# Optimization experiments

Hardware: AMD Instinct MI355X
Metric: run time of the kernel (lower is better)

Reference implementation:

```python
import math
import jax, jax.numpy as jnp
import numpy as np

B, T, D, DFF, E, K = 2, 4096, 1024, 2048, 8, 2
CAP_FACTOR = 1.25


def setup_inputs() -> dict:
    key = jax.random.key(0)
    ks = jax.random.split(key, 5)
    x = jax.random.normal(ks[0], (B, T, D), dtype=jnp.float32)
    gate_w = jax.random.normal(ks[1], (E, D), dtype=jnp.float32) * 0.02
    W1 = jax.random.normal(ks[2], (E, D, DFF), dtype=jnp.float32) * 0.02
    b1 = jnp.zeros((E, DFF), dtype=jnp.float32)
    W2 = jax.random.normal(ks[3], (E, DFF, D), dtype=jnp.float32) * 0.02
    b2 = jnp.zeros((E, D), dtype=jnp.float32)
    return {"x": x, "gate_w": gate_w, "W1": W1, "b1": b1, "W2": W2, "b2": b2}


def _moe_forward(x, gate_w, W1, b1, W2, b2):
    Bs, Ts, Ds = x.shape
    N = Bs * Ts
    x_flat = x.reshape(N, Ds)

    # --- router ---
    logits = x_flat @ gate_w.T                          # (N, E)
    probs = jax.nn.softmax(logits, axis=-1)             # (N, E)
    top_w, top_i = jax.lax.top_k(probs, K)              # (N, K)
    disp_w = top_w / (jnp.sum(top_w, axis=-1, keepdims=True) + 1e-9)

    # --- capacity: slot-major, token-order priority (matches the Python loops) ---
    capacity = max(1, int(math.ceil(CAP_FACTOR * N * K / E)))
    idx_flat = top_i.T.reshape(-1)                       # (K*N,) slot-major order
    oh = jax.nn.one_hot(idx_flat, E, dtype=jnp.int32)    # (K*N, E)
    # position of each assignment within its expert's arrival order
    pos = jnp.sum(jnp.cumsum(oh, axis=0) * oh, axis=-1) - 1  # (K*N,)
    keep = (pos < capacity).reshape(K, N).T              # (N, K)
    w_capped = disp_w * keep.astype(disp_w.dtype)        # (N, K)

    # --- combine weights per expert ---
    oh_nke = jax.nn.one_hot(top_i, E, dtype=w_capped.dtype)   # (N, K, E)
    comb = jnp.einsum('nk,nke->ne', w_capped, oh_nke)         # (N, E)

    # --- experts: dense per-expert FFN, zero-weight tokens contribute nothing ---
    out = jnp.zeros_like(x_flat)
    for e in range(E):
        h = jax.nn.gelu(x_flat @ W1[e] + b1[e], approximate=False)  # (N, DFF)
        y = h @ W2[e] + b2[e]                                        # (N, D)
        out = out + comb[:, e:e + 1] * y

    # --- Switch-style aux load-balancing loss ---
    assigned = (jnp.sum(oh_nke, axis=1) > 0).astype(probs.dtype)  # (N, E)
    f = jnp.mean(assigned, axis=0)
    p = jnp.mean(probs, axis=0)
    aux_loss = E * jnp.sum(f * p)

    return out.reshape(Bs, Ts, Ds), aux_loss


def reference(x, gate_w, W1, b1, W2, b2):
    return _moe_forward(x, gate_w, W1, b1, W2, b2)
```

## Files before the change

### kernel.cpp

```cpp
#include <hip/hip_runtime.h>
#include <hip/hip_bf16.h>
#include <math.h>

#define NB   2
#define NT   4096
#define ND   1024
#define NDFF 2048
#define NE   8
#define NK   2
#define NN   (NB * NT)
#define NCAP 2560

typedef unsigned short ushort_t;
typedef __attribute__((ext_vector_type(8))) short bf16x8;
typedef __attribute__((ext_vector_type(8))) unsigned short u16x8;
typedef __attribute__((ext_vector_type(4))) float f32x4;

__device__ __forceinline__ float gelu_exact(float v) {
  return 0.5f * v * (1.0f + erff(v * 0.70710678118654752f));
}

__device__ __forceinline__ unsigned short f2bf(float f) {
  unsigned int u = __float_as_uint(f);
  u += 0x7fffu + ((u >> 16) & 1u);
  return (unsigned short)(u >> 16);
}
__device__ __forceinline__ float bf2f(unsigned short h) {
  return __uint_as_float(((unsigned int)h) << 16);
}

__device__ __forceinline__ void gl_lds16(const void* g, void* l) {
  __builtin_amdgcn_global_load_lds(
      (__attribute__((address_space(1))) void*)g,
      (__attribute__((address_space(3))) void*)l, 16, 0, 0);
}

__global__ __launch_bounds__(256) void router_kernel(
    const float* __restrict__ x, const float* __restrict__ gw,
    int* __restrict__ top_i, float* __restrict__ disp_w,
    float* __restrict__ p_sum, int* __restrict__ f_cnt) {
  __shared__ float s_p[NE];
  __shared__ int s_f[NE];
  if (threadIdx.x < NE) { s_p[threadIdx.x] = 0.0f; s_f[threadIdx.x] = 0; }
  __syncthreads();

  const int lane = threadIdx.x & 63;
  const int wv = threadIdx.x >> 6;
  const int n = blockIdx.x * 4 + wv;

  const float4* xr = (const float4*)(x + (size_t)n * ND);
  float acc[NE];
#pragma unroll
  for (int e = 0; e < NE; ++e) acc[e] = 0.0f;

#pragma unroll
  for (int q = 0; q < 4; ++q) {
    float4 xv = xr[lane * 4 + q];
#pragma unroll
    for (int e = 0; e < NE; ++e) {
      float4 g = ((const float4*)(gw + (size_t)e * ND))[lane * 4 + q];
      acc[e] += xv.x * g.x + xv.y * g.y + xv.z * g.z + xv.w * g.w;
    }
  }
#pragma unroll
  for (int m = 1; m < 64; m <<= 1) {
#pragma unroll
    for (int e = 0; e < NE; ++e) acc[e] += __shfl_xor(acc[e], m, 64);
  }

  float mx = acc[0];
#pragma unroll
  for (int e = 1; e < NE; ++e) mx = fmaxf(mx, acc[e]);
  float p[NE];
  float s = 0.0f;
#pragma unroll
  for (int e = 0; e < NE; ++e) { p[e] = expf(acc[e] - mx); s += p[e]; }
  float inv = 1.0f / s;
#pragma unroll
  for (int e = 0; e < NE; ++e) p[e] *= inv;

  int i1 = 0; float v1 = p[0];
#pragma unroll
  for (int e = 1; e < NE; ++e) { if (p[e] > v1) { v1 = p[e]; i1 = e; } }
  int i2 = 0; float v2 = -1.0f;
#pragma unroll
  for (int e = 0; e < NE; ++e) { if (e != i1 && p[e] > v2) { v2 = p[e]; i2 = e; } }

  if (lane == 0) {
    float dsum = v1 + v2 + 1e-9f;
    top_i[n * NK + 0] = i1;
    top_i[n * NK + 1] = i2;
    disp_w[n * NK + 0] = v1 / dsum;
    disp_w[n * NK + 1] = v2 / dsum;
#pragma unroll
    for (int e = 0; e < NE; ++e) atomicAdd(&s_p[e], p[e]);
    atomicAdd(&s_f[i1], 1);
    atomicAdd(&s_f[i2], 1);
  }
  __syncthreads();
  if (threadIdx.x < NE) {
    atomicAdd(&p_sum[threadIdx.x], s_p[threadIdx.x]);
    atomicAdd(&f_cnt[threadIdx.x], s_f[threadIdx.x]);
  }
}

__global__ __launch_bounds__(512) void scan_kernel(
    const int* __restrict__ top_i, const float* __restrict__ disp_w,
    int* __restrict__ routed_tok, float* __restrict__ routed_w,
    int* __restrict__ counts, const float* __restrict__ p_sum,
    const int* __restrict__ f_cnt, float* __restrict__ aux_out) {
  __shared__ __align__(16) int s_top[NN * NK];
  for (int i = threadIdx.x; i < (NN * NK) / 4; i += 512)
    ((int4*)s_top)[i] = ((const int4*)top_i)[i];
  __syncthreads();

  const int e = threadIdx.x >> 6;
  const int lane = threadIdx.x & 63;
  int cnt = 0;
  for (int c = 0; c < (NN * NK) / 64; ++c) {
    int a = c * 64 + lane;
    int n = a & (NN - 1);
    int k = a >> 13;
    bool m = (s_top[n * NK + k] == e);
    unsigned long long mask = __ballot(m);
    if (m) {
      int pos = cnt + __popcll(mask & ((1ull << lane) - 1ull));
      if (pos < NCAP) {
        routed_tok[e * NCAP + pos] = n;
        routed_w[e * NCAP + pos] = disp_w[n * NK + k];
      }
    }
    cnt += (int)__popcll(mask);
  }
  if (lane == 0) counts[e] = (cnt < NCAP) ? cnt : NCAP;

  if (threadIdx.x == 0) {
    float aux = 0.0f;
    for (int j = 0; j < NE; ++j)
      aux += (p_sum[j] / (float)NN) * ((float)f_cnt[j] / (float)NN);
    aux_out[0] = aux * (float)NE;
  }
}

__global__ __launch_bounds__(256) void tsplit_kernel(
    const float* __restrict__ W, ushort_t* __restrict__ Thi,
    ushort_t* __restrict__ Tlo, int K, int N) {
  __shared__ float tile[64][65];
  const int t = threadIdx.x;
  const int n0 = blockIdx.x * 64, k0 = blockIdx.y * 64;
  {
    const int r = t >> 2, c16 = (t & 3) * 16;
    const float* src = W + (size_t)blockIdx.z * K * N +
                       (size_t)(k0 + r) * N + n0 + c16;
#pragma unroll
    for (int q = 0; q < 4; ++q) {
      float4 v = *(const float4*)(src + q * 4);
      tile[r][c16 + q * 4 + 0] = v.x;
      tile[r][c16 + q * 4 + 1] = v.y;
      tile[r][c16 + q * 4 + 2] = v.z;
      tile[r][c16 + q * 4 + 3] = v.w;
    }
  }
  __syncthreads();
  const int n = t >> 2, kc = (t & 3) * 16;
  u16x8 h0, h1, l0, l1;
#pragma unroll
  for (int j = 0; j < 8; ++j) {
    float f = tile[kc + j][n];
    unsigned short h = f2bf(f);
    h0[j] = h; l0[j] = f2bf(f - bf2f(h));
  }
#pragma unroll
  for (int j = 0; j < 8; ++j) {
    float f = tile[kc + 8 + j][n];
    unsigned short h = f2bf(f);
    h1[j] = h; l1[j] = f2bf(f - bf2f(h));
  }
  size_t o = (size_t)blockIdx.z * N * K + (size_t)(n0 + n) * K + k0 + kc;
  *(u16x8*)(Thi + o) = h0;
  *(u16x8*)(Thi + o + 8) = h1;
  *(u16x8*)(Tlo + o) = l0;
  *(u16x8*)(Tlo + o + 8) = l1;
}

__global__ __launch_bounds__(256, 3) void fgemm_fused(
    const float* __restrict__ x,
    const ushort_t* __restrict__ w1hi, const ushort_t* __restrict__ w1lo,
    const float* __restrict__ b1,
    const ushort_t* __restrict__ w2hi, const ushort_t* __restrict__ w2lo,
    const float* __restrict__ b2,
    const ushort_t* __restrict__ Hrhi, const ushort_t* __restrict__ Hrlo,
    ushort_t* __restrict__ Hwhi, ushort_t* __restrict__ Hwlo,
    const int* __restrict__ routed_tok, const float* __restrict__ routed_w,
    const int* __restrict__ counts, float* __restrict__ outf,
    int n_g1_z, int g1_lo, int g2_lo, int Rh) {
  const int bz = blockIdx.z;
  const bool isG1 = bz < n_g1_z;
  const int e = isG1 ? bz : bz - n_g1_z;
  const int count = counts[e];
  const int chunk_lo = isG1 ? g1_lo : g2_lo;
  const int local0 = blockIdx.y * 128;
  const int row0 = chunk_lo + local0;
  if (row0 >= count) return;
  const int bx = blockIdx.x;
  const int col0 = isG1 ? bx * 128 : (bx & 7) * 128;
  const int koff = isG1 ? 0 : (bx >> 3) * 1024;
  const int Ntot = isG1 ? NDFF : ND;
  const int Bstride = isG1 ? ND : NDFF;

  __shared__ __align__(16) char lds[32768];
  char* ldsA = lds;
  char* ldsB = lds + 16384;

  const int t = threadIdx.x;
  const int lane = t & 63;
  const int wid = t >> 6;
  const int wr = wid >> 1, wc = wid & 1;
  const int fr = lane & 15, ko = lane >> 4;

  const float* srcAf = nullptr;
  char* dstA[4] = {nullptr, nullptr, nullptr, nullptr};
  const ushort_t* srcA[4];
  if (isG1) {
    const int r = t >> 1, kp = (t & 1) * 2;
    const int rr = row0 + r;
    const int tok = routed_tok[e * NCAP + (rr < count ? rr : 0)];
    srcAf = x + (size_t)tok * ND + kp * 8;
    const int s = r & 7;
    dstA[0] = ldsA + (size_t)(r * 8 + ((kp + 0) ^ s)) * 16;
    dstA[1] = ldsA + (size_t)(r * 8 + ((kp + 1) ^ s)) * 16;
    dstA[2] = ldsA + (size_t)(r * 8 + ((kp + 4) ^ s)) * 16;
    dstA[3] = ldsA + (size_t)(r * 8 + ((kp + 5) ^ s)) * 16;
  } else {
#pragma unroll
    for (int c = 0; c < 4; ++c) {
      int ci = t + 256 * c;
      int r = ci >> 3, bp = ci & 7;
      int bs = bp ^ (r & 7);
      size_t arow = (size_t)e * Rh + local0 + r;
      srcA[c] = (bs < 4 ? Hrhi : Hrlo) + arow * (size_t)NDFF + koff + (bs & 3) * 8;
    }
  }
  const ushort_t* Bh = isG1 ? w1hi : w2hi;
  const ushort_t* Bl = isG1 ? w1lo : w2lo;
  const ushort_t* srcB[4];
#pragma unroll
  for (int c = 0; c < 4; ++c) {
    int ci = t + 256 * c;
    int cc = ci >> 3, bp = ci & 7;
    int bs = bp ^ (cc & 7);
    srcB[c] = (bs < 4 ? Bh : Bl) +
              ((size_t)e * Ntot + col0 + cc) * (size_t)Bstride + koff + (bs & 3) * 8;
  }

  f32x4 acc[4][4] = {};

  for (int ks = 0; ks < 1024; ks += 32) {
    if (isG1) {
      float4 v0 = *(const float4*)(srcAf);
      float4 v1 = *(const float4*)(srcAf + 4);
      float4 v2 = *(const float4*)(srcAf + 8);
      float4 v3 = *(const float4*)(srcAf + 12);
      srcAf += 32;
      u16x8 h0, h1, l0, l1;
      unsigned short h; float f;
      f = v0.x; h = f2bf(f); h0[0] = h; l0[0] = f2bf(f - bf2f(h));
      f = v0.y; h = f2bf(f); h0[1] = h; l0[1] = f2bf(f - bf2f(h));
      f = v0.z; h = f2bf(f); h0[2] = h; l0[2] = f2bf(f - bf2f(h));
      f = v0.w; h = f2bf(f); h0[3] = h; l0[3] = f2bf(f - bf2f(h));
      f = v1.x; h = f2bf(f); h0[4] = h; l0[4] = f2bf(f - bf2f(h));
      f = v1.y; h = f2bf(f); h0[5] = h; l0[5] = f2bf(f - bf2f(h));
      f = v1.z; h = f2bf(f); h0[6] = h; l0[6] = f2bf(f - bf2f(h));
      f = v1.w; h = f2bf(f); h0[7] = h; l0[7] = f2bf(f - bf2f(h));
      f = v2.x; h = f2bf(f); h1[0] = h; l1[0] = f2bf(f - bf2f(h));
      f = v2.y; h = f2bf(f); h1[1] = h; l1[1] = f2bf(f - bf2f(h));
      f = v2.z; h = f2bf(f); h1[2] = h; l1[2] = f2bf(f - bf2f(h));
      f = v2.w; h = f2bf(f); h1[3] = h; l1[3] = f2bf(f - bf2f(h));
      f = v3.x; h = f2bf(f); h1[4] = h; l1[4] = f2bf(f - bf2f(h));
      f = v3.y; h = f2bf(f); h1[5] = h; l1[5] = f2bf(f - bf2f(h));
      f = v3.z; h = f2bf(f); h1[6] = h; l1[6] = f2bf(f - bf2f(h));
      f = v3.w; h = f2bf(f); h1[7] = h; l1[7] = f2bf(f - bf2f(h));
      *(u16x8*)dstA[0] = h0;
      *(u16x8*)dstA[1] = h1;
      *(u16x8*)dstA[2] = l0;
      *(u16x8*)dstA[3] = l1;
    } else {
#pragma unroll
      for (int c = 0; c < 4; ++c) {
        gl_lds16(srcA[c], ldsA + (c * 256 + wid * 64) * 16);
        srcA[c] += 32;
      }
    }
#pragma unroll
    for (int c = 0; c < 4; ++c) {
      gl_lds16(srcB[c], ldsB + (c * 256 + wid * 64) * 16);
      srcB[c] += 32;
    }
    __syncthreads();

    bf16x8 Ah[4], Al[4], Bhf[4], Blf[4];
#pragma unroll
    for (int fi = 0; fi < 4; ++fi) {
      int r = wr * 64 + fi * 16 + fr;
      Ah[fi] = *(const bf16x8*)(ldsA + r * 128 + ((ko ^ (r & 7)) << 4));
      Al[fi] = *(const bf16x8*)(ldsA + r * 128 + (((4 + ko) ^ (r & 7)) << 4));
    }
#pragma unroll
    for (int fj = 0; fj < 4; ++fj) {
      int cc = wc * 64 + fj * 16 + fr;
      Bhf[fj] = *(const bf16x8*)(ldsB + cc * 128 + ((ko ^ (cc & 7)) << 4));
      Blf[fj] = *(const bf16x8*)(ldsB + cc * 128 + (((4 + ko) ^ (cc & 7)) << 4));
    }
#pragma unroll
    for (int fi = 0; fi < 4; ++fi)
#pragma unroll
      for (int fj = 0; fj < 4; ++fj) {
        acc[fi][fj] = __builtin_amdgcn_mfma_f32_16x16x32_bf16(
            Ah[fi], Bhf[fj], acc[fi][fj], 0, 0, 0);
        acc[fi][fj] = __builtin_amdgcn_mfma_f32_16x16x32_bf16(
            Ah[fi], Blf[fj], acc[fi][fj], 0, 0, 0);
        acc[fi][fj] = __builtin_amdgcn_mfma_f32_16x16x32_bf16(
            Al[fi], Bhf[fj], acc[fi][fj], 0, 0, 0);
      }
    __syncthreads();
  }

  const float* bias = isG1 ? b1 : b2;
  float bv[4];
#pragma unroll
  for (int fj = 0; fj < 4; ++fj)
    bv[fj] = (koff == 0)
                 ? bias[(size_t)e * Ntot + col0 + wc * 64 + fj * 16 + fr]
                 : 0.0f;

  if (isG1) {
#pragma unroll
    for (int fi = 0; fi < 4; ++fi) {
#pragma unroll
      for (int rg = 0; rg < 4; ++rg) {
        int rr = row0 + wr * 64 + fi * 16 + ko * 4 + rg;
        if (rr < count) {
          size_t rb = ((size_t)e * Rh + (rr - chunk_lo)) * (size_t)NDFF;
#pragma unroll
          for (int fj = 0; fj < 4; ++fj) {
            int cc = col0 + wc * 64 + fj * 16 + fr;
            float g = gelu_exact(acc[fi][fj][rg] + bv[fj]);
            unsigned short hh = f2bf(g);
            Hwhi[rb + cc] = hh;
            Hwlo[rb + cc] = f2bf(g - bf2f(hh));
          }
        }
      }
    }
  } else {
#pragma unroll
    for (int fi = 0; fi < 4; ++fi) {
#pragma unroll
      for (int rg = 0; rg < 4; ++rg) {
        int rr = row0 + wr * 64 + fi * 16 + ko * 4 + rg;
        if (rr < count) {
          int tok = routed_tok[e * NCAP + rr];
          float wgt = routed_w[e * NCAP + rr];
          float* orow = outf + (size_t)tok * ND;
#pragma unroll
          for (int fj = 0; fj < 4; ++fj) {
            int cc = col0 + wc * 64 + fj * 16 + fr;
            atomicAdd(orow + cc, wgt * (acc[fi][fj][rg] + bv[fj]));
          }
        }
      }
    }
  }
}

__global__ __launch_bounds__(256) void gemm1_kernel(
    const float* __restrict__ x, const float* __restrict__ W1,
    const float* __restrict__ b1, const int* __restrict__ routed_tok,
    const int* __restrict__ counts, float* __restrict__ H,
    int e0, size_t h_stride) {
  const int e = e0 + blockIdx.z;
  const int count = counts[e];
  const int row0 = blockIdx.y * 128;
  if (row0 >= count) return;
  const int col0 = blockIdx.x * 128;
  const float* W = W1 + (size_t)e * ND * NDFF;
  float* Hb = H + (size_t)blockIdx.z * h_stride;

  __shared__ __align__(16) float As[16][128];
  __shared__ __align__(16) float Bs[16][128];

  const int tid = threadIdx.x;
  const int arow = tid >> 1;
  const int aq = (tid & 1) * 8;
  const int r = row0 + arow;
  const int tok = routed_tok[e * NCAP + (r < count ? r : 0)];
  const float* Arow = x + (size_t)tok * ND;
  const int bk = tid >> 5;
  const int bc = (tid & 31) * 4;
  const int ty = tid >> 4, tx = tid & 15;

  float c[8][8] = {};

  for (int k0 = 0; k0 < ND; k0 += 16) {
    float4 av0 = *(const float4*)(Arow + k0 + aq);
    float4 av1 = *(const float4*)(Arow + k0 + aq + 4);
    float4 bv0 = *(const float4*)(W + (size_t)(k0 + bk) * NDFF + col0 + bc);
    float4 bv1 = *(const float4*)(W + (size_t)(k0 + bk + 8) * NDFF + col0 + bc);
    __syncthreads();
    As[aq + 0][arow] = av0.x; As[aq + 1][arow] = av0.y;
    As[aq + 2][arow] = av0.z; As[aq + 3][arow] = av0.w;
    As[aq + 4][arow] = av1.x; As[aq + 5][arow] = av1.y;
    As[aq + 6][arow] = av1.z; As[aq + 7][arow] = av1.w;
    *(float4*)&Bs[bk][bc] = bv0;
    *(float4*)&Bs[bk + 8][bc] = bv1;
    __syncthreads();
#pragma unroll
    for (int kk = 0; kk < 16; ++kk) {
      float4 a0 = *(const float4*)&As[kk][ty * 4];
      float4 a1 = *(const float4*)&As[kk][ty * 4 + 64];
      float4 b0 = *(const float4*)&Bs[kk][tx * 4];
      float4 b1r = *(const float4*)&Bs[kk][tx * 4 + 64];
      float ar[8] = {a0.x, a0.y, a0.z, a0.w, a1.x, a1.y, a1.z, a1.w};
      float br[8] = {b0.x, b0.y, b0.z, b0.w, b1r.x, b1r.y, b1r.z, b1r.w};
#pragma unroll
      for (int i = 0; i < 8; ++i)
#pragma unroll
        for (int j = 0; j < 8; ++j)
          c[i][j] = fmaf(ar[i], br[j], c[i][j]);
    }
  }

  const float* b1e = b1 + (size_t)e * NDFF + col0;
#pragma unroll
  for (int i = 0; i < 8; ++i) {
    int rr = row0 + ty * 4 + (i & 3) + (i >> 2) * 64;
    if (rr < count) {
      float* Hr = Hb + (size_t)rr * NDFF + col0;
      float4 v0, v1;
      v0.x = gelu_exact(c[i][0] + b1e[tx * 4 + 0]);
      v0.y = gelu_exact(c[i][1] + b1e[tx * 4 + 1]);
      v0.z = gelu_exact(c[i][2] + b1e[tx * 4 + 2]);
      v0.w = gelu_exact(c[i][3] + b1e[tx * 4 + 3]);
      v1.x = gelu_exact(c[i][4] + b1e[tx * 4 + 64]);
      v1.y = gelu_exact(c[i][5] + b1e[tx * 4 + 65]);
      v1.z = gelu_exact(c[i][6] + b1e[tx * 4 + 66]);
      v1.w = gelu_exact(c[i][7] + b1e[tx * 4 + 67]);
      *(float4*)(Hr + tx * 4) = v0;
      *(float4*)(Hr + tx * 4 + 64) = v1;
    }
  }
}

__global__ __launch_bounds__(256) void gemm2_kernel(
    const float* __restrict__ H, const float* __restrict__ W2,
    const float* __restrict__ b2, const int* __restrict__ routed_tok,
    const float* __restrict__ routed_w, const int* __restrict__ counts,
    float* __restrict__ out, int e0, size_t h_stride) {
  const int e = e0 + blockIdx.z;
  const int count = counts[e];
  const int row0 = blockIdx.y * 128;
  if (row0 >= count) return;
  const int col0 = blockIdx.x * 128;
  const float* W = W2 + (size_t)e * NDFF * ND;
  const float* Hb = H + (size_t)blockIdx.z * h_stride;

  __shared__ __align__(16) float As[16][128];
  __shared__ __align__(16) float Bs[16][128];

  const int tid = threadIdx.x;
  const int arow = tid >> 1;
  const int aq = (tid & 1) * 8;
  const float* Arow = Hb + (size_t)(row0 + arow) * NDFF;
  const int bk = tid >> 5;
  const int bc = (tid & 31) * 4;
  const int ty = tid >> 4, tx = tid & 15;

  float c[8][8] = {};

  for (int k0 = 0; k0 < NDFF; k0 += 16) {
    float4 av0 = *(const float4*)(Arow + k0 + aq);
    float4 av1 = *(const float4*)(Arow + k0 + aq + 4);
    float4 bv0 = *(const float4*)(W + (size_t)(k0 + bk) * ND + col0 + bc);
    float4 bv1 = *(const float4*)(W + (size_t)(k0 + bk + 8) * ND + col0 + bc);
    __syncthreads();
    As[aq + 0][arow] = av0.x; As[aq + 1][arow] = av0.y;
    As[aq + 2][arow] = av0.z; As[aq + 3][arow] = av0.w;
    As[aq + 4][arow] = av1.x; As[aq + 5][arow] = av1.y;
    As[aq + 6][arow] = av1.z; As[aq + 7][arow] = av1.w;
    *(float4*)&Bs[bk][bc] = bv0;
    *(float4*)&Bs[bk + 8][bc] = bv1;
    __syncthreads();
#pragma unroll
    for (int kk = 0; kk < 16; ++kk) {
      float4 a0 = *(const float4*)&As[kk][ty * 4];
      float4 a1 = *(const float4*)&As[kk][ty * 4 + 64];
      float4 b0 = *(const float4*)&Bs[kk][tx * 4];
      float4 b1r = *(const float4*)&Bs[kk][tx * 4 + 64];
      float ar[8] = {a0.x, a0.y, a0.z, a0.w, a1.x, a1.y, a1.z, a1.w};
      float br[8] = {b0.x, b0.y, b0.z, b0.w, b1r.x, b1r.y, b1r.z, b1r.w};
#pragma unroll
      for (int i = 0; i < 8; ++i)
#pragma unroll
        for (int j = 0; j < 8; ++j)
          c[i][j] = fmaf(ar[i], br[j], c[i][j]);
    }
  }

  const float* b2e = b2 + (size_t)e * ND + col0;
#pragma unroll
  for (int i = 0; i < 8; ++i) {
    int rr = row0 + ty * 4 + (i & 3) + (i >> 2) * 64;
    if (rr < count) {
      int tok = routed_tok[e * NCAP + rr];
      float wgt = routed_w[e * NCAP + rr];
      float* orow = out + (size_t)tok * ND + col0;
#pragma unroll
      for (int j = 0; j < 8; ++j) {
        int cc = tx * 4 + (j & 3) + (j >> 2) * 64;
        atomicAdd(orow + cc, wgt * (c[i][j] + b2e[cc]));
      }
    }
  }
}

extern "C" void kernel_launch(void* const* d_in, const int* in_sizes, int n_in,
                              void* d_out, int out_size, void* d_ws, size_t ws_size,
                              hipStream_t stream) {
  const float* x  = (const float*)d_in[0];
  const float* gw = (const float*)d_in[1];
  const float* W1 = (const float*)d_in[2];
  const float* b1 = (const float*)d_in[3];
  const float* W2 = (const float*)d_in[4];
  const float* b2 = (const float*)d_in[5];
  float* out = (float*)d_out;

  char* p = (char*)d_ws;
  auto alloc = [&](size_t bytes) -> char* {
    char* q = p;
    p += (bytes + 255) & ~(size_t)255;
    return q;
  };

  int*   top_i = (int*)alloc((size_t)NN * NK * 4);
  float* dispw = (float*)alloc((size_t)NN * NK * 4);
  int*   rtok  = (int*)alloc((size_t)NE * NCAP * 4);
  float* rw    = (float*)alloc((size_t)NE * NCAP * 4);
  int*   counts = (int*)alloc(256);
  float* psum  = (float*)alloc(64);
  int*   fcnt  = (int*)((char*)psum + 32);
  char*  p_base = p;

  hipMemsetAsync(out, 0, (size_t)NN * ND * 4, stream);
  hipMemsetAsync(psum, 0, 64, stream);

  router_kernel<<<NN / 4, 256, 0, stream>>>(x, gw, top_i, dispw, psum, fcnt);
  scan_kernel<<<1, 512, 0, stream>>>(top_i, dispw, rtok, rw, counts, psum, fcnt,
                                     out + (size_t)NN * ND);

  const size_t sw = (size_t)NE * ND * NDFF * 2;
  const size_t perRow = (size_t)NE * NDFF * 2 * 2;
  size_t wt_end = (size_t)(p_base - (char*)d_ws) + 4 * (sw + 256);
  size_t avail = (ws_size > wt_end + 8192) ? ws_size - wt_end - 8192 : 0;

  int Rh = 0;
  bool full = false;
  if (avail >= (size_t)NCAP * perRow) {
    full = true; Rh = NCAP;
  } else {
    Rh = (int)((avail / (2 * perRow)) & ~(size_t)127);
    if (Rh > NCAP - 128) Rh = NCAP - 128;
  }

  if (Rh >= 128) {
    ushort_t* w1hi = (ushort_t*)alloc(sw);
    ushort_t* w1lo = (ushort_t*)alloc(sw);
    ushort_t* w2hi = (ushort_t*)alloc(sw);
    ushort_t* w2lo = (ushort_t*)alloc(sw);

    tsplit_kernel<<<dim3(NDFF / 64, ND / 64, NE), 256, 0, stream>>>(
        W1, w1hi, w1lo, ND, NDFF);
    tsplit_kernel<<<dim3(ND / 64, NDFF / 64, NE), 256, 0, stream>>>(
        W2, w2hi, w2lo, NDFF, ND);

    const size_t hb = (size_t)NE * Rh * NDFF * 2;
    if (full) {
      ushort_t* Hhi = (ushort_t*)alloc(hb);
      ushort_t* Hlo = (ushort_t*)alloc(hb);
      fgemm_fused<<<dim3(16, NCAP / 128, 8), 256, 0, stream>>>(
          x, w1hi, w1lo, b1, w2hi, w2lo, b2, Hhi, Hlo, Hhi, Hlo,
          rtok, rw, counts, out, 8, 0, 0, Rh);
      fgemm_fused<<<dim3(16, NCAP / 128, 8), 256, 0, stream>>>(
          x, w1hi, w1lo, b1, w2hi, w2lo, b2, Hhi, Hlo, Hhi, Hlo,
          rtok, rw, counts, out, 0, 0, 0, Rh);
    } else {
      ushort_t* h0hi = (ushort_t*)alloc(hb);
      ushort_t* h0lo = (ushort_t*)alloc(hb);
      ushort_t* h1hi = (ushort_t*)alloc(hb);
      ushort_t* h1lo = (ushort_t*)alloc(hb);
      ushort_t* bh[2] = {h0hi, h1hi};
      ushort_t* bl[2] = {h0lo, h1lo};
      const int P = (NCAP + Rh - 1) / Rh;
      const int ylen = Rh / 128;
      fgemm_fused<<<dim3(16, ylen, 8), 256, 0, stream>>>(
          x, w1hi, w1lo, b1, w2hi, w2lo, b2, bh[0], bl[0], bh[0], bl[0],
          rtok, rw, counts, out, 8, 0, 0, Rh);
      for (int i = 1; i < P; ++i) {
        fgemm_fused<<<dim3(16, ylen, 16), 256, 0, stream>>>(
            x, w1hi, w1lo, b1, w2hi, w2lo, b2,
            bh[(i - 1) & 1], bl[(i - 1) & 1], bh[i & 1], bl[i & 1],
            rtok, rw, counts, out, 8, i * Rh, (i - 1) * Rh, Rh);
      }
      fgemm_fused<<<dim3(16, ylen, 8), 256, 0, stream>>>(
          x, w1hi, w1lo, b1, w2hi, w2lo, b2,
          bh[(P - 1) & 1], bl[(P - 1) & 1], bh[(P - 1) & 1], bl[(P - 1) & 1],
          rtok, rw, counts, out, 0, 0, (P - 1) * Rh, Rh);
    }
  } else {
    p = p_base;
    float* H = (float*)p;
    const size_t need_old_full =
        (size_t)(p_base - (char*)d_ws) + (size_t)NE * NCAP * NDFF * 4 + 8192;
    const bool fullH = (ws_size >= need_old_full);
    if (fullH) {
      gemm1_kernel<<<dim3(NDFF / 128, NCAP / 128, NE), 256, 0, stream>>>(
          x, W1, b1, rtok, counts, H, 0, (size_t)NCAP * NDFF);
      gemm2_kernel<<<dim3(ND / 128, NCAP / 128, NE), 256, 0, stream>>>(
          H, W2, b2, rtok, rw, counts, out, 0, (size_t)NCAP * NDFF);
    } else {
      for (int e = 0; e < NE; ++e) {
        gemm1_kernel<<<dim3(NDFF / 128, NCAP / 128, 1), 256, 0, stream>>>(
            x, W1, b1, rtok, counts, H, e, 0);
        gemm2_kernel<<<dim3(ND / 128, NCAP / 128, 1), 256, 0, stream>>>(
            H, W2, b2, rtok, rw, counts, out, e, 0);
      }
    }
  }
}
```

Baseline: 967.1 us.

## Overlap next K-tile global loads with MFMA compute in expert GEMM loop

The main K loop is restructured so the first tile is loaded before the loop. Each iteration reads fragments from LDS, hits a barrier, and then issues the global/LDS loads for the next tile before running the MFMAs. For the G1 path, the fp32 to bf16 hi/lo conversion and LDS write happen after the MFMAs. This is meant to hide global memory latency behind the matrix math while keeping a single LDS buffer. The cost is register pressure from holding the prefetched float4 values, plus a dependence on barrier placement for correctness.

```diff
diff --git a/kernel.cpp b/kernel.cpp
--- a/kernel.cpp
+++ b/kernel.cpp
@@ -253,50 +253,56 @@
               ((size_t)e * Ntot + col0 + cc) * (size_t)Bstride + koff + (bs & 3) * 8;
   }
 
+  auto cvt_write = [&](float4 v0, float4 v1, float4 v2, float4 v3) {
+    u16x8 h0, h1, l0, l1;
+    unsigned short h; float f;
+    f = v0.x; h = f2bf(f); h0[0] = h; l0[0] = f2bf(f - bf2f(h));
+    f = v0.y; h = f2bf(f); h0[1] = h; l0[1] = f2bf(f - bf2f(h));
+    f = v0.z; h = f2bf(f); h0[2] = h; l0[2] = f2bf(f - bf2f(h));
+    f = v0.w; h = f2bf(f); h0[3] = h; l0[3] = f2bf(f - bf2f(h));
+    f = v1.x; h = f2bf(f); h0[4] = h; l0[4] = f2bf(f - bf2f(h));
+    f = v1.y; h = f2bf(f); h0[5] = h; l0[5] = f2bf(f - bf2f(h));
+    f = v1.z; h = f2bf(f); h0[6] = h; l0[6] = f2bf(f - bf2f(h));
+    f = v1.w; h = f2bf(f); h0[7] = h; l0[7] = f2bf(f - bf2f(h));
+    f = v2.x; h = f2bf(f); h1[0] = h; l1[0] = f2bf(f - bf2f(h));
+    f = v2.y; h = f2bf(f); h1[1] = h; l1[1] = f2bf(f - bf2f(h));
+    f = v2.z; h = f2bf(f); h1[2] = h; l1[2] = f2bf(f - bf2f(h));
+    f = v2.w; h = f2bf(f); h1[3] = h; l1[3] = f2bf(f - bf2f(h));
+    f = v3.x; h = f2bf(f); h1[4] = h; l1[4] = f2bf(f - bf2f(h));
+    f = v3.y; h = f2bf(f); h1[5] = h; l1[5] = f2bf(f - bf2f(h));
+    f = v3.z; h = f2bf(f); h1[6] = h; l1[6] = f2bf(f - bf2f(h));
+    f = v3.w; h = f2bf(f); h1[7] = h; l1[7] = f2bf(f - bf2f(h));
+    *(u16x8*)dstA[0] = h0;
+    *(u16x8*)dstA[1] = h1;
+    *(u16x8*)dstA[2] = l0;
+    *(u16x8*)dstA[3] = l1;
+  };
+
+  if (isG1) {
+    float4 p0 = *(const float4*)(srcAf);
+    float4 p1 = *(const float4*)(srcAf + 4);
+    float4 p2 = *(const float4*)(srcAf + 8);
+    float4 p3 = *(const float4*)(srcAf + 12);
+    srcAf += 32;
+    cvt_write(p0, p1, p2, p3);
+  } else {
+#pragma unroll
+    for (int c = 0; c < 4; ++c) {
+      gl_lds16(srcA[c], ldsA + (c * 256 + wid * 64) * 16);
+      srcA[c] += 32;
+    }
+  }
+#pragma unroll
+  for (int c = 0; c < 4; ++c) {
+    gl_lds16(srcB[c], ldsB + (c * 256 + wid * 64) * 16);
+    srcB[c] += 32;
+  }
+  __syncthreads();
+
   f32x4 acc[4][4] = {};
 
   for (int ks = 0; ks < 1024; ks += 32) {
-    if (isG1) {
-      float4 v0 = *(const float4*)(srcAf);
-      float4 v1 = *(const float4*)(srcAf + 4);
-      float4 v2 = *(const float4*)(srcAf + 8);
-      float4 v3 = *(const float4*)(srcAf + 12);
-      srcAf += 32;
-      u16x8 h0, h1, l0, l1;
-      unsigned short h; float f;
-      f = v0.x; h = f2bf(f); h0[0] = h; l0[0] = f2bf(f - bf2f(h));
-      f = v0.y; h = f2bf(f); h0[1] = h; l0[1] = f2bf(f - bf2f(h));
-      f = v0.z; h = f2bf(f); h0[2] = h; l0[2] = f2bf(f - bf2f(h));
-      f = v0.w; h = f2bf(f); h0[3] = h; l0[3] = f2bf(f - bf2f(h));
-      f = v1.x; h = f2bf(f); h0[4] = h; l0[4] = f2bf(f - bf2f(h));
-      f = v1.y; h = f2bf(f); h0[5] = h; l0[5] = f2bf(f - bf2f(h));
-      f = v1.z; h = f2bf(f); h0[6] = h; l0[6] = f2bf(f - bf2f(h));
-      f = v1.w; h = f2bf(f); h0[7] = h; l0[7] = f2bf(f - bf2f(h));
-      f = v2.x; h = f2bf(f); h1[0] = h; l1[0] = f2bf(f - bf2f(h));
-      f = v2.y; h = f2bf(f); h1[1] = h; l1[1] = f2bf(f - bf2f(h));
-      f = v2.z; h = f2bf(f); h1[2] = h; l1[2] = f2bf(f - bf2f(h));
-      f = v2.w; h = f2bf(f); h1[3] = h; l1[3] = f2bf(f - bf2f(h));
-      f = v3.x; h = f2bf(f); h1[4] = h; l1[4] = f2bf(f - bf2f(h));
-      f = v3.y; h = f2bf(f); h1[5] = h; l1[5] = f2bf(f - bf2f(h));
-      f = v3.z; h = f2bf(f); h1[6] = h; l1[6] = f2bf(f - bf2f(h));
-      f = v3.w; h = f2bf(f); h1[7] = h; l1[7] = f2bf(f - bf2f(h));
-      *(u16x8*)dstA[0] = h0;
-      *(u16x8*)dstA[1] = h1;
-      *(u16x8*)dstA[2] = l0;
-      *(u16x8*)dstA[3] = l1;
-    } else {
-#pragma unroll
-      for (int c = 0; c < 4; ++c) {
-        gl_lds16(srcA[c], ldsA + (c * 256 + wid * 64) * 16);
-        srcA[c] += 32;
-      }
-    }
-#pragma unroll
-    for (int c = 0; c < 4; ++c) {
-      gl_lds16(srcB[c], ldsB + (c * 256 + wid * 64) * 16);
-      srcB[c] += 32;
-    }
-    __syncthreads();
+    const bool notlast = (ks < 1024 - 32);
 
     bf16x8 Ah[4], Al[4], Bhf[4], Blf[4];
 #pragma unroll
@@ -311,6 +317,30 @@
       Bhf[fj] = *(const bf16x8*)(ldsB + cc * 128 + ((ko ^ (cc & 7)) << 4));
       Blf[fj] = *(const bf16x8*)(ldsB + cc * 128 + (((4 + ko) ^ (cc & 7)) << 4));
     }
+
+    float4 v0, v1, v2, v3;
+    if (notlast) {
+      __syncthreads();
+      if (isG1) {
+        v0 = *(const float4*)(srcAf);
+        v1 = *(const float4*)(srcAf + 4);
+        v2 = *(const float4*)(srcAf + 8);
+        v3 = *(const float4*)(srcAf + 12);
+        srcAf += 32;
+      } else {
+#pragma unroll
+        for (int c = 0; c < 4; ++c) {
+          gl_lds16(srcA[c], ldsA + (c * 256 + wid * 64) * 16);
+          srcA[c] += 32;
+        }
+      }
+#pragma unroll
+      for (int c = 0; c < 4; ++c) {
+        gl_lds16(srcB[c], ldsB + (c * 256 + wid * 64) * 16);
+        srcB[c] += 32;
+      }
+    }
+
 #pragma unroll
     for (int fi = 0; fi < 4; ++fi)
 #pragma unroll
@@ -322,7 +352,11 @@
         acc[fi][fj] = __builtin_amdgcn_mfma_f32_16x16x32_bf16(
             Al[fi], Bhf[fj], acc[fi][fj], 0, 0, 0);
       }
-    __syncthreads();
+
+    if (notlast) {
+      if (isG1) cvt_write(v0, v1, v2, v3);
+      __syncthreads();
+    }
   }
 
   const float* bias = isG1 ? b1 : b2;
```

Measured after the change: 1.510 ms. 56.1% more time.
